# Performance work log

Measured on AMD Instinct MI355X. Metric: run time of the kernel, lower is better.

The kernel has to match this reference:

```python
import jax, jax.numpy as jnp
import numpy as np

D_MODEL = 1024
D_FF = 2048
N_EXPERTS = 8
Z_LOSS_COEF = 0.001


def setup_inputs() -> dict:
    key = jax.random.key(0)
    kx, kr, k1, k3, k2 = jax.random.split(key, 5)
    s_in = 1.0 / np.sqrt(D_MODEL)
    s_ff = 1.0 / np.sqrt(D_FF)
    return {
        "x": jax.random.normal(kx, (4, 2048, D_MODEL), dtype=jnp.float32),
        # router: nn.Linear(d_model, num_experts, bias=False) -> weight [E, D]
        "Wr": jax.random.normal(kr, (N_EXPERTS, D_MODEL), dtype=jnp.float32) * s_in,
        # stacked expert weights, torch Linear layout [out, in]
        "W1": jax.random.normal(k1, (N_EXPERTS, D_FF, D_MODEL), dtype=jnp.float32) * s_in,
        "W3": jax.random.normal(k3, (N_EXPERTS, D_FF, D_MODEL), dtype=jnp.float32) * s_in,
        "W2": jax.random.normal(k2, (N_EXPERTS, D_MODEL, D_FF), dtype=jnp.float32) * s_ff,
    }


def reference(x, Wr, W1, W3, W2):
    B, S, D = x.shape
    E = Wr.shape[0]
    xf = x.reshape(B * S, D)          # [T, D]
    T = xf.shape[0]

    # --- router ---
    logits = xf @ Wr.T                # [T, E]
    probs = jax.nn.softmax(logits, axis=-1)
    top2_p, top2_i = jax.lax.top_k(probs, 2)          # [T, 2]
    top2_p = top2_p / (jnp.sum(top2_p, axis=-1, keepdims=True) + 1e-9)

    # dense gate matrix: zero for unselected experts (same math as index_add combine)
    gates = jnp.zeros((T, E), jnp.float32).at[jnp.arange(T)[:, None], top2_i].add(top2_p)

    # --- experts (SwiGLU), computed per-expert over all tokens, masked by gates ---
    h1 = jax.nn.silu(jnp.einsum('td,efd->etf', xf, W1))   # [E, T, F]
    h3 = jnp.einsum('td,efd->etf', xf, W3)                 # [E, T, F]
    y = jnp.einsum('etf,edf->etd', h1 * h3, W2)            # [E, T, D]
    out = jnp.einsum('etd,te->td', y.astype(jnp.float32), gates)
    out = out.astype(x.dtype).reshape(B, S, D)

    # --- losses ---
    z = jax.nn.logsumexp(logits.astype(jnp.float32), axis=-1)
    router_loss = Z_LOSS_COEF * jnp.mean(z * z)

    importance = jnp.sum(probs.astype(jnp.float32), axis=0) / T   # [E]
    top1 = top2_i[:, 0]
    load = jnp.zeros((E,), jnp.float32).at[top1].add(1.0) / T
    aux_loss = jnp.sum(importance * load) * E

    return out, router_loss, aux_loss
```

## Files before the change

### kernel.cpp

```cpp
#include <hip/hip_runtime.h>
#include <stdint.h>

#define NT 8192
#define DM 1024
#define DF 2048
#define RT_BLOCKS 256

typedef __attribute__((ext_vector_type(8))) short short8;
typedef __attribute__((ext_vector_type(4))) float f32x4;
typedef unsigned short us;

__device__ __forceinline__ us f2bf(float f) {
  uint32_t x = __float_as_uint(f);
  return (us)((x + 0x7fffu + ((x >> 16) & 1u)) >> 16);
}
__device__ __forceinline__ float bf2f(us v) {
  return __uint_as_float(((uint32_t)v) << 16);
}

__device__ __forceinline__ void gload16(const void* g, void* l) {
  __builtin_amdgcn_global_load_lds(
      (const __attribute__((address_space(1))) uint32_t*)g,
      (__attribute__((address_space(3))) uint32_t*)l, 16, 0, 0);
}

__global__ void k_cvtw(const float4* __restrict__ w1, const float4* __restrict__ w3,
                       const float4* __restrict__ w2,
                       short8* __restrict__ w13, short8* __restrict__ w2bf) {
  int s = blockIdx.y;
  const float4* src = (s == 0) ? w1 : (s == 1) ? w3 : w2;
  int n8 = 8 * DF * DM / 8;
  int i = blockIdx.x * blockDim.x + threadIdx.x;
  int st = gridDim.x * blockDim.x;
  for (; i < n8; i += st) {
    float4 va = src[2 * i], vb = src[2 * i + 1];
    short8 o;
    o[0] = (short)f2bf(va.x); o[1] = (short)f2bf(va.y);
    o[2] = (short)f2bf(va.z); o[3] = (short)f2bf(va.w);
    o[4] = (short)f2bf(vb.x); o[5] = (short)f2bf(vb.y);
    o[6] = (short)f2bf(vb.z); o[7] = (short)f2bf(vb.w);
    if (s == 2) {
      w2bf[i] = o;
    } else {
      int e = i >> 18;
      int rem = i & ((1 << 18) - 1);
      int f = rem >> 7;
      int k8 = rem & 127;
      int n = 32 * (f >> 4) + 16 * s + (f & 15);
      w13[((size_t)e << 19) + (size_t)n * 128 + k8] = o;
    }
  }
}

__global__ void k_router(const float* __restrict__ x, const float* __restrict__ wr,
                         int* cntb, int* cnt1, float* imp, float* z2,
                         int* epack, float2* gts, us* __restrict__ xbf) {
  int lane = threadIdx.x & 63;
  int wid = threadIdx.x >> 6;
  const float4* w4 = (const float4*)wr;

  float imp_acc[8] = {0.f, 0.f, 0.f, 0.f, 0.f, 0.f, 0.f, 0.f};
  float z2_acc = 0.f;
  int cb_acc[8] = {0, 0, 0, 0, 0, 0, 0, 0};
  int c1_acc[8] = {0, 0, 0, 0, 0, 0, 0, 0};

  for (int t = blockIdx.x * 4 + wid; t < NT; t += RT_BLOCKS * 4) {
    const float4* x4 = (const float4*)(x + (size_t)t * DM);
    ushort4* xb4 = (ushort4*)(xbf + (size_t)t * DM);
    float4 xv[4];
    #pragma unroll
    for (int j = 0; j < 4; ++j) {
      xv[j] = x4[lane + 64 * j];
      ushort4 o;
      o.x = f2bf(xv[j].x); o.y = f2bf(xv[j].y); o.z = f2bf(xv[j].z); o.w = f2bf(xv[j].w);
      xb4[lane + 64 * j] = o;
    }
    float p[8];
    #pragma unroll
    for (int e = 0; e < 8; ++e) p[e] = 0.f;
    #pragma unroll
    for (int j = 0; j < 4; ++j) {
      #pragma unroll
      for (int e = 0; e < 8; ++e) {
        float4 wv = w4[e * 256 + lane + 64 * j];
        p[e] += xv[j].x * wv.x + xv[j].y * wv.y + xv[j].z * wv.z + xv[j].w * wv.w;
      }
    }
    #pragma unroll
    for (int off = 32; off > 0; off >>= 1) {
      #pragma unroll
      for (int e = 0; e < 8; ++e) p[e] += __shfl_down(p[e], off);
    }
    if (lane == 0) {
      float m = p[0];
      #pragma unroll
      for (int e = 1; e < 8; ++e) m = fmaxf(m, p[e]);
      float pr[8], sum = 0.f;
      #pragma unroll
      for (int e = 0; e < 8; ++e) { pr[e] = expf(p[e] - m); sum += pr[e]; }
      float inv = 1.f / sum;
      #pragma unroll
      for (int e = 0; e < 8; ++e) pr[e] *= inv;
      float z = m + logf(sum);
      int e0 = 0; float b0 = p[0];
      #pragma unroll
      for (int e = 1; e < 8; ++e) { if (p[e] > b0) { b0 = p[e]; e0 = e; } }
      int e1 = -1; float b1 = -1e30f;
      #pragma unroll
      for (int e = 0; e < 8; ++e) { if (e != e0 && p[e] > b1) { b1 = p[e]; e1 = e; } }
      float p0 = 0.f, p1 = 0.f;
      #pragma unroll
      for (int e = 0; e < 8; ++e) {
        p0 = (e == e0) ? pr[e] : p0;
        p1 = (e == e1) ? pr[e] : p1;
      }
      float gs = p0 + p1 + 1e-9f;
      epack[t] = e0 | (e1 << 16);
      gts[t] = make_float2(p0 / gs, p1 / gs);
      z2_acc += z * z;
      #pragma unroll
      for (int e = 0; e < 8; ++e) {
        imp_acc[e] += pr[e];
        cb_acc[e] += (e == e0) + (e == e1);
        c1_acc[e] += (e == e0);
      }
    }
  }

  __shared__ float simp[4][8];
  __shared__ float sz2[4];
  __shared__ int scb[4][8];
  __shared__ int sc1[4][8];
  if (lane == 0) {
    #pragma unroll
    for (int e = 0; e < 8; ++e) { simp[wid][e] = imp_acc[e]; scb[wid][e] = cb_acc[e]; sc1[wid][e] = c1_acc[e]; }
    sz2[wid] = z2_acc;
  }
  __syncthreads();
  int tid = threadIdx.x;
  if (tid < 8) {
    float ss = simp[0][tid] + simp[1][tid] + simp[2][tid] + simp[3][tid];
    int b = scb[0][tid] + scb[1][tid] + scb[2][tid] + scb[3][tid];
    int o = sc1[0][tid] + sc1[1][tid] + sc1[2][tid] + sc1[3][tid];
    atomicAdd(&imp[tid], ss);
    atomicAdd(&cntb[tid], b);
    atomicAdd(&cnt1[tid], o);
  } else if (tid == 8) {
    atomicAdd(z2, sz2[0] + sz2[1] + sz2[2] + sz2[3]);
  }
}

__global__ void k_finalize(const int* cntb, const int* cnt1, const float* imp,
                           const float* z2, int* offs, float* otail) {
  if (threadIdx.x == 0 && blockIdx.x == 0) {
    int o = 0;
    for (int e = 0; e < 8; ++e) { offs[e] = o; o += cntb[e]; }
    otail[0] = 1e-3f * z2[0] / (float)NT;
    float aux = 0.f;
    for (int e = 0; e < 8; ++e)
      aux += (imp[e] / (float)NT) * ((float)cnt1[e] / (float)NT);
    otail[1] = aux * 8.f;
  }
}

__global__ void k_scatter(const int* __restrict__ epack, const float2* __restrict__ gts,
                          const int* __restrict__ offs,
                          int* __restrict__ btok, int* __restrict__ pos) {
  int e = blockIdx.x;
  int lane = threadIdx.x;
  int base = offs[e];
  int run = 0;
  for (int j0 = 0; j0 < 2 * NT; j0 += 64) {
    int j = j0 + lane;
    int t = j >> 1;
    int ep = epack[t];
    int sel = (j & 1) ? (ep >> 16) : (ep & 0xffff);
    bool f = (sel == e);
    unsigned long long m = __ballot(f);
    int rank = __popcll(m & ((1ull << lane) - 1ull));
    if (f) {
      int slot = base + run + rank;
      btok[slot] = t;
      pos[j] = slot;
    }
    run += __popcll(m);
  }
}


__global__ __launch_bounds__(256) void k_ffn1(
    const us* __restrict__ xb, const us* __restrict__ w13,
    const int* __restrict__ offs, const int* __restrict__ cnts,
    const int* __restrict__ btok, us* __restrict__ hg) {
  int e = blockIdx.z;
  int cnt = cnts[e];
  int m0 = blockIdx.y * 128;
  if (m0 >= cnt) return;
  int n0 = blockIdx.x * 128;
  int off = offs[e];
  __shared__ __align__(16) short As[2][4096];
  __shared__ __align__(16) short Bs[2][4096];
  __shared__ int tok[128];
  int tid = threadIdx.x, lane = tid & 63, wid = tid >> 6;
  if (tid < 128) {
    int r = m0 + tid; if (r > cnt - 1) r = cnt - 1;
    tok[tid] = btok[off + r];
  }
  __syncthreads();

  int prow = tid >> 3;
  int pu = (tid & 7) ^ (prow & 7);
  int row0 = prow * 2 + (pu >> 2);
  int gc = (pu & 3) * 8;
  const us* w13e = w13 + ((size_t)e << 22);
  const us* a0 = xb + (size_t)tok[row0] * DM + gc;
  const us* a1 = xb + (size_t)tok[row0 + 64] * DM + gc;
  const us* b0 = w13e + (size_t)(n0 + row0) * DM + gc;
  const us* b1 = w13e + (size_t)(n0 + row0 + 64) * DM + gc;
  int dsl = tid * 8;

  int wm = wid >> 1, wn = wid & 1;
  int fr = lane & 15, glog = lane >> 4;
  int pos = (((fr & 1) << 2) | glog) ^ ((fr >> 1) & 7);
  int aoff = (wm * 32 + (fr >> 1)) * 64 + pos * 8;
  int boff = (wn * 32 + (fr >> 1)) * 64 + pos * 8;
  f32x4 acc[4][4] = {};

  const int NK = DM / 64;
  for (int kt = 0; kt < NK; ++kt) {
    int k0 = kt * 64;
    #pragma unroll
    for (int h = 0; h < 2; ++h) {
      int ko = k0 + h * 32;
      gload16(a0 + ko, &As[h][dsl]);
      gload16(a1 + ko, &As[h][dsl + 2048]);
      gload16(b0 + ko, &Bs[h][dsl]);
      gload16(b1 + ko, &Bs[h][dsl + 2048]);
    }
    __syncthreads();
    #pragma unroll
    for (int h = 0; h < 2; ++h) {
      short8 a[4], b[4];
      #pragma unroll
      for (int mi = 0; mi < 4; ++mi) a[mi] = *(const short8*)&As[h][aoff + mi * 512];
      #pragma unroll
      for (int ni = 0; ni < 4; ++ni) b[ni] = *(const short8*)&Bs[h][boff + ni * 512];
      #pragma unroll
      for (int mi = 0; mi < 4; ++mi) {
        #pragma unroll
        for (int ni = 0; ni < 4; ++ni)
          acc[mi][ni] = __builtin_amdgcn_mfma_f32_16x16x32_bf16(a[mi], b[ni], acc[mi][ni], 0, 0, 0);
      }
    }
    __syncthreads();
  }

  int c = lane & 15, r4 = (lane >> 4) * 4;
  int fb = (n0 + wn * 64) >> 1;
  #pragma unroll
  for (int mi = 0; mi < 4; ++mi) {
    #pragma unroll
    for (int rg = 0; rg < 4; ++rg) {
      int gr = m0 + wm * 64 + mi * 16 + r4 + rg;
      if (gr < cnt) {
        us* hrow = hg + (size_t)(off + gr) * DF;
        #pragma unroll
        for (int j = 0; j < 2; ++j) {
          float a1v = acc[mi][2 * j][rg];
          float a3v = acc[mi][2 * j + 1][rg];
          float h = (a1v / (1.f + __expf(-a1v))) * a3v;
          hrow[fb + j * 16 + c] = f2bf(h);
        }
      }
    }
  }
}

__global__ __launch_bounds__(256) void k_ffn2(
    const us* __restrict__ hg, const us* __restrict__ w2b,
    const int* __restrict__ offs, const int* __restrict__ cnts,
    us* __restrict__ ys) {
  int e = blockIdx.z;
  int cnt = cnts[e];
  int m0 = blockIdx.y * 128;
  if (m0 >= cnt) return;
  int n0 = blockIdx.x * 128;
  int off = offs[e];
  __shared__ __align__(16) short As[2][4096];
  __shared__ __align__(16) short Bs[2][4096];
  int tid = threadIdx.x, lane = tid & 63, wid = tid >> 6;

  int prow = tid >> 3;
  int pu = (tid & 7) ^ (prow & 7);
  int row0 = prow * 2 + (pu >> 2);
  int gc = (pu & 3) * 8;
  int ar0 = m0 + row0;      if (ar0 > cnt - 1) ar0 = cnt - 1;
  int ar1 = m0 + row0 + 64; if (ar1 > cnt - 1) ar1 = cnt - 1;
  const us* w2e = w2b + ((size_t)e << 21);
  const us* a0 = hg + (size_t)(off + ar0) * DF + gc;
  const us* a1 = hg + (size_t)(off + ar1) * DF + gc;
  const us* b0 = w2e + (size_t)(n0 + row0) * DF + gc;
  const us* b1 = w2e + (size_t)(n0 + row0 + 64) * DF + gc;
  int dsl = tid * 8;

  int wm = wid >> 1, wn = wid & 1;
  int fr = lane & 15, glog = lane >> 4;
  int pos = (((fr & 1) << 2) | glog) ^ ((fr >> 1) & 7);
  int aoff = (wm * 32 + (fr >> 1)) * 64 + pos * 8;
  int boff = (wn * 32 + (fr >> 1)) * 64 + pos * 8;
  f32x4 acc[4][4] = {};

  const int NK = DF / 64;
  for (int kt = 0; kt < NK; ++kt) {
    int k0 = kt * 64;
    #pragma unroll
    for (int h = 0; h < 2; ++h) {
      int ko = k0 + h * 32;
      gload16(a0 + ko, &As[h][dsl]);
      gload16(a1 + ko, &As[h][dsl + 2048]);
      gload16(b0 + ko, &Bs[h][dsl]);
      gload16(b1 + ko, &Bs[h][dsl + 2048]);
    }
    __syncthreads();
    #pragma unroll
    for (int h = 0; h < 2; ++h) {
      short8 a[4], b[4];
      #pragma unroll
      for (int mi = 0; mi < 4; ++mi) a[mi] = *(const short8*)&As[h][aoff + mi * 512];
      #pragma unroll
      for (int ni = 0; ni < 4; ++ni) b[ni] = *(const short8*)&Bs[h][boff + ni * 512];
      #pragma unroll
      for (int mi = 0; mi < 4; ++mi) {
        #pragma unroll
        for (int ni = 0; ni < 4; ++ni)
          acc[mi][ni] = __builtin_amdgcn_mfma_f32_16x16x32_bf16(a[mi], b[ni], acc[mi][ni], 0, 0, 0);
      }
    }
    __syncthreads();
  }

  int c = lane & 15, r4 = (lane >> 4) * 4;
  #pragma unroll
  for (int mi = 0; mi < 4; ++mi) {
    #pragma unroll
    for (int rg = 0; rg < 4; ++rg) {
      int gr = m0 + wm * 64 + mi * 16 + r4 + rg;
      if (gr < cnt) {
        us* yrow = ys + (size_t)(off + gr) * DM + n0;
        #pragma unroll
        for (int ni = 0; ni < 4; ++ni)
          yrow[wn * 64 + ni * 16 + c] = f2bf(acc[mi][ni][rg]);
      }
    }
  }
}

__global__ void k_gather(const us* __restrict__ ys, const int* __restrict__ pos,
                         const float2* __restrict__ gts, float* __restrict__ out) {
  int idx = blockIdx.x * blockDim.x + threadIdx.x;
  int t = idx >> 8;
  int d4 = idx & 255;
  float2 g = gts[t];
  ushort4 a = ((const ushort4*)(ys + (size_t)pos[2 * t] * DM))[d4];
  ushort4 b = ((const ushort4*)(ys + (size_t)pos[2 * t + 1] * DM))[d4];
  float4 o;
  o.x = g.x * bf2f(a.x) + g.y * bf2f(b.x);
  o.y = g.x * bf2f(a.y) + g.y * bf2f(b.y);
  o.z = g.x * bf2f(a.z) + g.y * bf2f(b.z);
  o.w = g.x * bf2f(a.w) + g.y * bf2f(b.w);
  ((float4*)out)[idx] = o;
}


extern "C" void kernel_launch(void* const* d_in, const int* in_sizes, int n_in,
                              void* d_out, int out_size, void* d_ws, size_t ws_size,
                              hipStream_t stream) {
  const float* x  = (const float*)d_in[0];
  const float* wr = (const float*)d_in[1];
  const float* w1 = (const float*)d_in[2];
  const float* w3 = (const float*)d_in[3];
  const float* w2 = (const float*)d_in[4];
  float* out = (float*)d_out;

  uint8_t* ws = (uint8_t*)d_ws;
  int*    cntb   = (int*)(ws + 0);
  int*    cnt1   = (int*)(ws + 32);
  int*    offs   = (int*)(ws + 96);
  float*  imp    = (float*)(ws + 128);
  float*  z2     = (float*)(ws + 160);
  int*    epack  = (int*)(ws + 4096);
  float2* gts    = (float2*)(ws + 36864);
  int*    btok   = (int*)(ws + 102400);
  int*    pos    = (int*)(ws + 167936);
  us*     xbf    = (us*)(ws + 233472);
  us*     w13    = (us*)(ws + 17010688);
  us*     w2bf   = (us*)(ws + 84119552);
  us*     hg     = (us*)(ws + 117673984);
  us*     ysb    = (us*)(ws + 17010688);

  hipMemsetAsync(ws, 0, 4096, stream);

  k_router<<<RT_BLOCKS, 256, 0, stream>>>(x, wr, cntb, cnt1, imp, z2, epack, gts, xbf);
  k_cvtw<<<dim3(2048, 3), 256, 0, stream>>>(
      (const float4*)w1, (const float4*)w3, (const float4*)w2,
      (short8*)w13, (short8*)w2bf);

  k_finalize<<<1, 64, 0, stream>>>(cntb, cnt1, imp, z2, offs, out + (size_t)NT * DM);
  k_scatter<<<8, 64, 0, stream>>>(epack, gts, offs, btok, pos);

  k_ffn1<<<dim3(32, 128, 8), 256, 0, stream>>>(xbf, w13, offs, cntb, btok, hg);
  k_ffn2<<<dim3(8, 128, 8), 256, 0, stream>>>(hg, w2bf, offs, cntb, ysb);
  k_gather<<<NT * DM / 4 / 256, 256, 0, stream>>>(ysb, pos, gts, out);
}
```

Measured before the change: 503.7 us.

## Use persistent grouped-GEMM with compact work list; merge finalize into scatter

The finalize and scatter kernels are merged so one kernel computes offsets and losses and also builds a compact list of (expert, m-tile) work items. The FFN kernels become persistent grids of 1024 blocks that loop over this list, replacing grids of 32x128x8 and 8x128x8 blocks where most blocks exited early. This removes one launch and the scheduling cost of many empty blocks. In exchange, each block processes tiles one after another without overlap between tiles, and the work list is built serially by a single thread.

```diff
diff --git a/kernel.cpp b/kernel.cpp
--- a/kernel.cpp
+++ b/kernel.cpp
@@ -150,24 +150,31 @@
   }
 }
 
-__global__ void k_finalize(const int* cntb, const int* cnt1, const float* imp,
-                           const float* z2, int* offs, float* otail) {
-  if (threadIdx.x == 0 && blockIdx.x == 0) {
-    int o = 0;
-    for (int e = 0; e < 8; ++e) { offs[e] = o; o += cntb[e]; }
+__global__ void k_scatter2(const int* __restrict__ cntb, const int* __restrict__ cnt1,
+                           const float* __restrict__ imp, const float* __restrict__ z2,
+                           const int* __restrict__ epack,
+                           int* __restrict__ offs_g, float* __restrict__ otail,
+                           int* __restrict__ btok, int* __restrict__ pos,
+                           int* __restrict__ wl, int* __restrict__ nwork) {
+  int e = blockIdx.x;
+  int lane = threadIdx.x;
+  int offs[8]; int o = 0;
+  #pragma unroll
+  for (int i = 0; i < 8; ++i) { offs[i] = o; o += cntb[i]; }
+  if (e == 0 && lane == 0) {
+    #pragma unroll
+    for (int i = 0; i < 8; ++i) offs_g[i] = offs[i];
     otail[0] = 1e-3f * z2[0] / (float)NT;
     float aux = 0.f;
-    for (int e = 0; e < 8; ++e)
-      aux += (imp[e] / (float)NT) * ((float)cnt1[e] / (float)NT);
+    for (int i = 0; i < 8; ++i)
+      aux += (imp[i] / (float)NT) * ((float)cnt1[i] / (float)NT);
     otail[1] = aux * 8.f;
-  }
-}
-
-__global__ void k_scatter(const int* __restrict__ epack, const float2* __restrict__ gts,
-                          const int* __restrict__ offs,
-                          int* __restrict__ btok, int* __restrict__ pos) {
-  int e = blockIdx.x;
-  int lane = threadIdx.x;
+    int np = 0;
+    for (int i = 0; i < 8; ++i)
+      for (int m = 0; m * 128 < cntb[i]; ++m)
+        wl[np++] = (i << 16) | m;
+    nwork[0] = np;
+  }
   int base = offs[e];
   int run = 0;
   for (int j0 = 0; j0 < 2 * NT; j0 += 64) {
@@ -190,86 +197,93 @@
 
 __global__ __launch_bounds__(256) void k_ffn1(
     const us* __restrict__ xb, const us* __restrict__ w13,
-    const int* __restrict__ offs, const int* __restrict__ cnts,
-    const int* __restrict__ btok, us* __restrict__ hg) {
-  int e = blockIdx.z;
-  int cnt = cnts[e];
-  int m0 = blockIdx.y * 128;
-  if (m0 >= cnt) return;
-  int n0 = blockIdx.x * 128;
-  int off = offs[e];
+    const int* __restrict__ offs_g, const int* __restrict__ cnts,
+    const int* __restrict__ btok, const int* __restrict__ wl,
+    const int* __restrict__ nwork, us* __restrict__ hg) {
   __shared__ __align__(16) short As[2][4096];
   __shared__ __align__(16) short Bs[2][4096];
   __shared__ int tok[128];
   int tid = threadIdx.x, lane = tid & 63, wid = tid >> 6;
-  if (tid < 128) {
-    int r = m0 + tid; if (r > cnt - 1) r = cnt - 1;
-    tok[tid] = btok[off + r];
-  }
-  __syncthreads();
 
   int prow = tid >> 3;
   int pu = (tid & 7) ^ (prow & 7);
   int row0 = prow * 2 + (pu >> 2);
   int gc = (pu & 3) * 8;
-  const us* w13e = w13 + ((size_t)e << 22);
-  const us* a0 = xb + (size_t)tok[row0] * DM + gc;
-  const us* a1 = xb + (size_t)tok[row0 + 64] * DM + gc;
-  const us* b0 = w13e + (size_t)(n0 + row0) * DM + gc;
-  const us* b1 = w13e + (size_t)(n0 + row0 + 64) * DM + gc;
   int dsl = tid * 8;
-
   int wm = wid >> 1, wn = wid & 1;
   int fr = lane & 15, glog = lane >> 4;
   int pos = (((fr & 1) << 2) | glog) ^ ((fr >> 1) & 7);
   int aoff = (wm * 32 + (fr >> 1)) * 64 + pos * 8;
   int boff = (wn * 32 + (fr >> 1)) * 64 + pos * 8;
-  f32x4 acc[4][4] = {};
-
-  const int NK = DM / 64;
-  for (int kt = 0; kt < NK; ++kt) {
-    int k0 = kt * 64;
-    #pragma unroll
-    for (int h = 0; h < 2; ++h) {
-      int ko = k0 + h * 32;
-      gload16(a0 + ko, &As[h][dsl]);
-      gload16(a1 + ko, &As[h][dsl + 2048]);
-      gload16(b0 + ko, &Bs[h][dsl]);
-      gload16(b1 + ko, &Bs[h][dsl + 2048]);
-    }
+  int c = lane & 15, r4 = (lane >> 4) * 4;
+
+  int nw = nwork[0] * 32;
+  for (int w = blockIdx.x; w < nw; w += gridDim.x) {
+    int pr = wl[w >> 5];
+    int e = pr >> 16;
+    int m0 = (pr & 0xffff) * 128;
+    int n0 = (w & 31) * 128;
+    int cnt = cnts[e];
+    int off = offs_g[e];
+
     __syncthreads();
-    #pragma unroll
-    for (int h = 0; h < 2; ++h) {
-      short8 a[4], b[4];
-      #pragma unroll
-      for (int mi = 0; mi < 4; ++mi) a[mi] = *(const short8*)&As[h][aoff + mi * 512];
-      #pragma unroll
-      for (int ni = 0; ni < 4; ++ni) b[ni] = *(const short8*)&Bs[h][boff + ni * 512];
-      #pragma unroll
-      for (int mi = 0; mi < 4; ++mi) {
-        #pragma unroll
-        for (int ni = 0; ni < 4; ++ni)
-          acc[mi][ni] = __builtin_amdgcn_mfma_f32_16x16x32_bf16(a[mi], b[ni], acc[mi][ni], 0, 0, 0);
-      }
+    if (tid < 128) {
+      int r = m0 + tid; if (r > cnt - 1) r = cnt - 1;
+      tok[tid] = btok[off + r];
     }
     __syncthreads();
-  }
-
-  int c = lane & 15, r4 = (lane >> 4) * 4;
-  int fb = (n0 + wn * 64) >> 1;
-  #pragma unroll
-  for (int mi = 0; mi < 4; ++mi) {
-    #pragma unroll
-    for (int rg = 0; rg < 4; ++rg) {
-      int gr = m0 + wm * 64 + mi * 16 + r4 + rg;
-      if (gr < cnt) {
-        us* hrow = hg + (size_t)(off + gr) * DF;
-        #pragma unroll
-        for (int j = 0; j < 2; ++j) {
-          float a1v = acc[mi][2 * j][rg];
-          float a3v = acc[mi][2 * j + 1][rg];
-          float h = (a1v / (1.f + __expf(-a1v))) * a3v;
-          hrow[fb + j * 16 + c] = f2bf(h);
+
+    const us* w13e = w13 + ((size_t)e << 22);
+    const us* a0 = xb + (size_t)tok[row0] * DM + gc;
+    const us* a1 = xb + (size_t)tok[row0 + 64] * DM + gc;
+    const us* b0 = w13e + (size_t)(n0 + row0) * DM + gc;
+    const us* b1 = w13e + (size_t)(n0 + row0 + 64) * DM + gc;
+    f32x4 acc[4][4] = {};
+
+    const int NK = DM / 64;
+    for (int kt = 0; kt < NK; ++kt) {
+      int k0 = kt * 64;
+      #pragma unroll
+      for (int h = 0; h < 2; ++h) {
+        int ko = k0 + h * 32;
+        gload16(a0 + ko, &As[h][dsl]);
+        gload16(a1 + ko, &As[h][dsl + 2048]);
+        gload16(b0 + ko, &Bs[h][dsl]);
+        gload16(b1 + ko, &Bs[h][dsl + 2048]);
+      }
+      __syncthreads();
+      #pragma unroll
+      for (int h = 0; h < 2; ++h) {
+        short8 a[4], b[4];
+        #pragma unroll
+        for (int mi = 0; mi < 4; ++mi) a[mi] = *(const short8*)&As[h][aoff + mi * 512];
+        #pragma unroll
+        for (int ni = 0; ni < 4; ++ni) b[ni] = *(const short8*)&Bs[h][boff + ni * 512];
+        #pragma unroll
+        for (int mi = 0; mi < 4; ++mi) {
+          #pragma unroll
+          for (int ni = 0; ni < 4; ++ni)
+            acc[mi][ni] = __builtin_amdgcn_mfma_f32_16x16x32_bf16(a[mi], b[ni], acc[mi][ni], 0, 0, 0);
+        }
+      }
+      __syncthreads();
+    }
+
+    int fb = (n0 + wn * 64) >> 1;
+    #pragma unroll
+    for (int mi = 0; mi < 4; ++mi) {
+      #pragma unroll
+      for (int rg = 0; rg < 4; ++rg) {
+        int gr = m0 + wm * 64 + mi * 16 + r4 + rg;
+        if (gr < cnt) {
+          us* hrow = hg + (size_t)(off + gr) * DF;
+          #pragma unroll
+          for (int j = 0; j < 2; ++j) {
+            float a1v = acc[mi][2 * j][rg];
+            float a3v = acc[mi][2 * j + 1][rg];
+            float h = (a1v / (1.f + __expf(-a1v))) * a3v;
+            hrow[fb + j * 16 + c] = f2bf(h);
+          }
         }
       }
     }
@@ -278,14 +292,9 @@
 
 __global__ __launch_bounds__(256) void k_ffn2(
     const us* __restrict__ hg, const us* __restrict__ w2b,
-    const int* __restrict__ offs, const int* __restrict__ cnts,
+    const int* __restrict__ offs_g, const int* __restrict__ cnts,
+    const int* __restrict__ wl, const int* __restrict__ nwork,
     us* __restrict__ ys) {
-  int e = blockIdx.z;
-  int cnt = cnts[e];
-  int m0 = blockIdx.y * 128;
-  if (m0 >= cnt) return;
-  int n0 = blockIdx.x * 128;
-  int off = offs[e];
   __shared__ __align__(16) short As[2][4096];
   __shared__ __align__(16) short Bs[2][4096];
   int tid = threadIdx.x, lane = tid & 63, wid = tid >> 6;
@@ -294,62 +303,73 @@
   int pu = (tid & 7) ^ (prow & 7);
   int row0 = prow * 2 + (pu >> 2);
   int gc = (pu & 3) * 8;
-  int ar0 = m0 + row0;      if (ar0 > cnt - 1) ar0 = cnt - 1;
-  int ar1 = m0 + row0 + 64; if (ar1 > cnt - 1) ar1 = cnt - 1;
-  const us* w2e = w2b + ((size_t)e << 21);
-  const us* a0 = hg + (size_t)(off + ar0) * DF + gc;
-  const us* a1 = hg + (size_t)(off + ar1) * DF + gc;
-  const us* b0 = w2e + (size_t)(n0 + row0) * DF + gc;
-  const us* b1 = w2e + (size_t)(n0 + row0 + 64) * DF + gc;
   int dsl = tid * 8;
-
   int wm = wid >> 1, wn = wid & 1;
   int fr = lane & 15, glog = lane >> 4;
   int pos = (((fr & 1) << 2) | glog) ^ ((fr >> 1) & 7);
   int aoff = (wm * 32 + (fr >> 1)) * 64 + pos * 8;
   int boff = (wn * 32 + (fr >> 1)) * 64 + pos * 8;
-  f32x4 acc[4][4] = {};
-
-  const int NK = DF / 64;
-  for (int kt = 0; kt < NK; ++kt) {
-    int k0 = kt * 64;
-    #pragma unroll
-    for (int h = 0; h < 2; ++h) {
-      int ko = k0 + h * 32;
-      gload16(a0 + ko, &As[h][dsl]);
-      gload16(a1 + ko, &As[h][dsl + 2048]);
-      gload16(b0 + ko, &Bs[h][dsl]);
-      gload16(b1 + ko, &Bs[h][dsl + 2048]);
-    }
+  int c = lane & 15, r4 = (lane >> 4) * 4;
+
+  int nw = nwork[0] * 8;
+  for (int w = blockIdx.x; w < nw; w += gridDim.x) {
+    int pr = wl[w >> 3];
+    int e = pr >> 16;
+    int m0 = (pr & 0xffff) * 128;
+    int n0 = (w & 7) * 128;
+    int cnt = cnts[e];
+    int off = offs_g[e];
+
+    int ar0 = m0 + row0;      if (ar0 > cnt - 1) ar0 = cnt - 1;
+    int ar1 = m0 + row0 + 64; if (ar1 > cnt - 1) ar1 = cnt - 1;
+    const us* w2e = w2b + ((size_t)e << 21);
+    const us* a0 = hg + (size_t)(off + ar0) * DF + gc;
+    const us* a1 = hg + (size_t)(off + ar1) * DF + gc;
+    const us* b0 = w2e + (size_t)(n0 + row0) * DF + gc;
+    const us* b1 = w2e + (size_t)(n0 + row0 + 64) * DF + gc;
+    f32x4 acc[4][4] = {};
+
     __syncthreads();
-    #pragma unroll
-    for (int h = 0; h < 2; ++h) {
-      short8 a[4], b[4];
-      #pragma unroll
-      for (int mi = 0; mi < 4; ++mi) a[mi] = *(const short8*)&As[h][aoff + mi * 512];
-      #pragma unroll
-      for (int ni = 0; ni < 4; ++ni) b[ni] = *(const short8*)&Bs[h][boff + ni * 512];
-      #pragma unroll
-      for (int mi = 0; mi < 4; ++mi) {
-        #pragma unroll
-        for (int ni = 0; ni < 4; ++ni)
-          acc[mi][ni] = __builtin_amdgcn_mfma_f32_16x16x32_bf16(a[mi], b[ni], acc[mi][ni], 0, 0, 0);
-      }
-    }
-    __syncthreads();
-  }
-
-  int c = lane & 15, r4 = (lane >> 4) * 4;
-  #pragma unroll
-  for (int mi = 0; mi < 4; ++mi) {
-    #pragma unroll
-    for (int rg = 0; rg < 4; ++rg) {
-      int gr = m0 + wm * 64 + mi * 16 + r4 + rg;
-      if (gr < cnt) {
-        us* yrow = ys + (size_t)(off + gr) * DM + n0;
-        #pragma unroll
-        for (int ni = 0; ni < 4; ++ni)
-          yrow[wn * 64 + ni * 16 + c] = f2bf(acc[mi][ni][rg]);
+    const int NK = DF / 64;
+    for (int kt = 0; kt < NK; ++kt) {
+      int k0 = kt * 64;
+      #pragma unroll
+      for (int h = 0; h < 2; ++h) {
+        int ko = k0 + h * 32;
+        gload16(a0 + ko, &As[h][dsl]);
+        gload16(a1 + ko, &As[h][dsl + 2048]);
+        gload16(b0 + ko, &Bs[h][dsl]);
+        gload16(b1 + ko, &Bs[h][dsl + 2048]);
+      }
+      __syncthreads();
+      #pragma unroll
+      for (int h = 0; h < 2; ++h) {
+        short8 a[4], b[4];
+        #pragma unroll
+        for (int mi = 0; mi < 4; ++mi) a[mi] = *(const short8*)&As[h][aoff + mi * 512];
+        #pragma unroll
+        for (int ni = 0; ni < 4; ++ni) b[ni] = *(const short8*)&Bs[h][boff + ni * 512];
+        #pragma unroll
+        for (int mi = 0; mi < 4; ++mi) {
+          #pragma unroll
+          for (int ni = 0; ni < 4; ++ni)
+            acc[mi][ni] = __builtin_amdgcn_mfma_f32_16x16x32_bf16(a[mi], b[ni], acc[mi][ni], 0, 0, 0);
+        }
+      }
+      __syncthreads();
+    }
+
+    #pragma unroll
+    for (int mi = 0; mi < 4; ++mi) {
+      #pragma unroll
+      for (int rg = 0; rg < 4; ++rg) {
+        int gr = m0 + wm * 64 + mi * 16 + r4 + rg;
+        if (gr < cnt) {
+          us* yrow = ys + (size_t)(off + gr) * DM + n0;
+          #pragma unroll
+          for (int ni = 0; ni < 4; ++ni)
+            yrow[wn * 64 + ni * 16 + c] = f2bf(acc[mi][ni][rg]);
+        }
       }
     }
   }
@@ -388,6 +408,8 @@
   int*    offs   = (int*)(ws + 96);
   float*  imp    = (float*)(ws + 128);
   float*  z2     = (float*)(ws + 160);
+  int*    nwork  = (int*)(ws + 192);
+  int*    wl     = (int*)(ws + 1024);
   int*    epack  = (int*)(ws + 4096);
   float2* gts    = (float2*)(ws + 36864);
   int*    btok   = (int*)(ws + 102400);
@@ -405,10 +427,10 @@
       (const float4*)w1, (const float4*)w3, (const float4*)w2,
       (short8*)w13, (short8*)w2bf);
 
-  k_finalize<<<1, 64, 0, stream>>>(cntb, cnt1, imp, z2, offs, out + (size_t)NT * DM);
-  k_scatter<<<8, 64, 0, stream>>>(epack, gts, offs, btok, pos);
-
-  k_ffn1<<<dim3(32, 128, 8), 256, 0, stream>>>(xbf, w13, offs, cntb, btok, hg);
-  k_ffn2<<<dim3(8, 128, 8), 256, 0, stream>>>(hg, w2bf, offs, cntb, ysb);
+  k_scatter2<<<8, 64, 0, stream>>>(cntb, cnt1, imp, z2, epack,
+                                   offs, out + (size_t)NT * DM, btok, pos, wl, nwork);
+
+  k_ffn1<<<1024, 256, 0, stream>>>(xbf, w13, offs, cntb, btok, wl, nwork, hg);
+  k_ffn2<<<1024, 256, 0, stream>>>(hg, w2bf, offs, cntb, wl, nwork, ysb);
   k_gather<<<NT * DM / 4 / 256, 256, 0, stream>>>(ysb, pos, gts, out);
 }
```

New measurement: 564.9 us. 12.1% more time.
